# Performance work log

Hardware: AMD Instinct MI355X
Metric: run time of the kernel (lower is better)

## Reference

```python
import jax, jax.numpy as jnp
import numpy as np
import math


def setup_inputs() -> dict:
    key = jax.random.key(0)
    B, H, CL, QL = 16, 128, 2048, 256
    k0, k1, k2 = jax.random.split(key, 3)
    context = jax.random.normal(k0, (B, H, CL), dtype=jnp.float32)
    question = jax.random.normal(k1, (B, H, QL), dtype=jnp.float32)
    c_mask = jnp.ones((B, CL), dtype=jnp.int32)
    q_mask = jnp.ones((B, QL), dtype=jnp.int32)
    lim = math.sqrt(1.0 / H)
    w = jax.random.uniform(k2, (3 * H,), minval=-lim, maxval=lim, dtype=jnp.float32)
    return {"context": context, "question": question, "c_mask": c_mask, "q_mask": q_mask, "w": w}


def reference(context, question, c_mask, q_mask, w):
    # context: (B, H, c_len), question: (B, H, q_len), w: (3H,)
    H = context.shape[1]
    ctx = jnp.transpose(context, (0, 2, 1))   # (B, c_len, H)
    qry = jnp.transpose(question, (0, 2, 1))  # (B, q_len, H)
    wq, wc, wcq = w[:H], w[H:2 * H], w[2 * H:]
    # Trilinear similarity computed directly (no (B,c,q,3H) materialization):
    # s[b,i,j] = wq.q_j + wc.c_i + wcq.(c_i*q_j); torch layout after transpose is (B, c_len, q_len)
    s = (ctx @ wc)[:, :, None] + (qry @ wq)[:, None, :] + jnp.einsum('bch,bqh->bcq', ctx * wcq, qry)
    NEG = jnp.float32(-1e30)
    s1 = jax.nn.softmax(jnp.where(q_mask[:, None, :] > 0, s, NEG), axis=2)  # softmax over q
    s2 = jax.nn.softmax(jnp.where(c_mask[:, :, None] > 0, s, NEG), axis=1)  # softmax over c
    a = jnp.einsum('bcq,bqh->bch', s1, qry)          # context-to-query attention
    l = jnp.einsum('bcq,bkq->bck', s1, s2)           # s1 @ s2^T, (B, c_len, c_len)
    b = jnp.einsum('bck,bkh->bch', l, ctx)           # query-to-context attention
    out = jnp.concatenate([ctx, a, ctx * a, ctx * b], axis=2)  # (B, c_len, 4H)
    # drop_prob=0 -> dropout is identity
    return jnp.transpose(out, (0, 2, 1))  # (B, 4H, c_len)
```

## Files before the change

### kernel.cpp

```cpp
#include <hip/hip_runtime.h>

typedef short bf16x8 __attribute__((ext_vector_type(8)));
typedef float f32x16 __attribute__((ext_vector_type(16)));
typedef float f32x4  __attribute__((ext_vector_type(4)));

constexpr int B  = 16;
constexpr int H  = 128;
constexpr int CL = 2048;
constexpr int QL = 256;
constexpr int SPLITK5 = 8;
constexpr int K5SEG = CL / SPLITK5;
constexpr float SHIFT = 8.0f;

__device__ __forceinline__ unsigned short f2bf(float x) {
  unsigned u = __float_as_uint(x);
  u += 0x7fffu + ((u >> 16) & 1u);
  return (unsigned short)(u >> 16);
}
__device__ __forceinline__ float bf2f(unsigned short u) {
  return __uint_as_float((unsigned)u << 16);
}

template<int L, bool SCALE, bool WOUT, bool CM>
__device__ __forceinline__ void ktrans_body(
    const float* __restrict__ src, const float* __restrict__ wbias,
    const float* __restrict__ wscale, const int* __restrict__ cmask,
    unsigned short* __restrict__ dlin, unsigned short* __restrict__ dT,
    unsigned short* __restrict__ dm,
    float* __restrict__ pbias, float* __restrict__ outg0,
    int bxl, int h1, int b, int tid,
    unsigned short (*T)[72], float (*P)[64]) {
  const int c0 = bxl * 64;
  const int hh = tid >> 4;
  const int cc4 = (tid & 15) * 4;
  int4 cm4;
  if (CM) cm4 = *(const int4*)&cmask[b * L + c0 + cc4];
  float4 part = make_float4(0.f, 0.f, 0.f, 0.f);
  #pragma unroll
  for (int it = 0; it < 4; ++it) {
    const int hrow = it * 16 + hh;
    const int h = h1 * 64 + hrow;
    float4 v = *(const float4*)&src[((size_t)b * H + h) * L + c0 + cc4];
    const float wb = wbias[h];
    part.x = fmaf(v.x, wb, part.x); part.y = fmaf(v.y, wb, part.y);
    part.z = fmaf(v.z, wb, part.z); part.w = fmaf(v.w, wb, part.w);
    if (WOUT) {
      f32x4 t;
      t[0] = v.x; t[1] = v.y; t[2] = v.z; t[3] = v.w;
      __builtin_nontemporal_store(
          t, (f32x4*)&outg0[((size_t)b * 4 * H + h) * (size_t)CL + c0 + cc4]);
    }
    ushort4 o;
    o.x = f2bf(v.x); o.y = f2bf(v.y); o.z = f2bf(v.z); o.w = f2bf(v.w);
    *(ushort4*)&dlin[((size_t)b * H + h) * L + c0 + cc4] = o;
    if (CM) {
      ushort4 om;
      om.x = cm4.x > 0 ? o.x : (unsigned short)0;
      om.y = cm4.y > 0 ? o.y : (unsigned short)0;
      om.z = cm4.z > 0 ? o.z : (unsigned short)0;
      om.w = cm4.w > 0 ? o.w : (unsigned short)0;
      *(ushort4*)&dm[((size_t)b * H + h) * L + c0 + cc4] = om;
    }
    ushort4 ot;
    if (SCALE) {
      const float ws = wscale[h];
      ot.x = f2bf(v.x * ws); ot.y = f2bf(v.y * ws);
      ot.z = f2bf(v.z * ws); ot.w = f2bf(v.w * ws);
    } else {
      ot = o;
    }
    *(ushort4*)&T[hrow][cc4] = ot;
  }
  *(float4*)&P[hh][cc4] = part;
  __syncthreads();
  if (tid < 64) {
    float sum = 0.f;
    #pragma unroll
    for (int i = 0; i < 16; ++i) sum += P[i][tid];
    pbias[(size_t)h1 * B * L + (size_t)b * L + c0 + tid] = sum;
  }
  #pragma unroll
  for (int it = 0; it < 4; ++it) {
    int lin = it * 256 + tid;
    int c = lin >> 4, hc = (lin & 15) * 4;
    ushort4 o;
    o.x = T[hc + 0][c]; o.y = T[hc + 1][c];
    o.z = T[hc + 2][c]; o.w = T[hc + 3][c];
    *(ushort4*)&dT[((size_t)b * L + c0 + c) * H + h1 * 64 + hc] = o;
  }
}

__global__ __launch_bounds__(256) void ktrans_all(
    const float* __restrict__ ctx, const float* __restrict__ qry,
    const float* __restrict__ w, const int* __restrict__ cmask,
    unsigned short* __restrict__ ctx_bf, unsigned short* __restrict__ ctxwT,
    unsigned short* __restrict__ ctxm,
    unsigned short* __restrict__ qry_bf, unsigned short* __restrict__ qryT,
    float* __restrict__ pct, float* __restrict__ pqt,
    float* __restrict__ out) {
  __shared__ unsigned short T[64][72];
  __shared__ float P[16][64];
  const int h1 = blockIdx.y, b = blockIdx.z, tid = threadIdx.x;
  const int bx = blockIdx.x;
  if (bx < CL / 64) {
    ktrans_body<CL, true, true, true>(ctx, w + H, w + 2 * H, cmask,
                                      ctx_bf, ctxwT, ctxm, pct, out,
                                      bx, h1, b, tid, T, P);
  } else {
    ktrans_body<QL, false, false, false>(qry, w, w, nullptr,
                                         qry_bf, qryT, nullptr, pqt, nullptr,
                                         bx - CL / 64, h1, b, tid, T, P);
  }
}

__global__ __launch_bounds__(512) void k2_score3(
    const unsigned short* __restrict__ ctxwT, const unsigned short* __restrict__ qryT,
    const float* __restrict__ pct, const float* __restrict__ pqt,
    const int* __restrict__ cmask, const int* __restrict__ qmask,
    unsigned short* __restrict__ eu,
    float* __restrict__ rsum_g, float* __restrict__ Lpart) {
  __shared__ unsigned short t2[256 * 40];
  __shared__ float stats[32][8];
  __shared__ float cmf[32];
  const int wg = blockIdx.x;
  const int b = wg & (B - 1);
  const int cblk = wg >> 4;
  const int c0 = cblk * 32;
  const int tid = threadIdx.x;
  const int w = tid >> 6;
  const int l = tid & 63;
  const int lr = l & 31, hi = l >> 5;
  const int q0 = w * 32;
  const int c = c0 + lr;

  if (tid < 32) cmf[tid] = cmask[b * CL + c0 + tid] > 0 ? 1.f : 0.f;

  const unsigned short* ap = qryT + ((size_t)b * QL + q0 + lr) * H + hi * 8;
  const unsigned short* bp = ctxwT + ((size_t)b * CL + c) * H + hi * 8;
  f32x16 acc = {};
  #pragma unroll
  for (int k = 0; k < H; k += 16) {
    bf16x8 af = *(const bf16x8*)(ap + k);
    bf16x8 bf_ = *(const bf16x8*)(bp + k);
    acc = __builtin_amdgcn_mfma_f32_32x32x16_bf16(af, bf_, acc, 0, 0, 0);
  }

  const float ct = pct[b * CL + c] + pct[B * CL + b * CL + c];

  float rs = 0.f;
  #pragma unroll
  for (int g = 0; g < 4; ++g) {
    const int qbase = q0 + 4 * hi + 8 * g;
    float4 qa = *(const float4*)&pqt[b * QL + qbase];
    float4 qb = *(const float4*)&pqt[B * QL + b * QL + qbase];
    int4 m4 = *(const int4*)&qmask[b * QL + qbase];
    float e0 = __expf(acc[4 * g + 0] + ct + qa.x + qb.x - SHIFT);
    float e1 = __expf(acc[4 * g + 1] + ct + qa.y + qb.y - SHIFT);
    float e2 = __expf(acc[4 * g + 2] + ct + qa.z + qb.z - SHIFT);
    float e3 = __expf(acc[4 * g + 3] + ct + qa.w + qb.w - SHIFT);
    rs += (m4.x > 0 ? e0 : 0.f) + (m4.y > 0 ? e1 : 0.f) +
          (m4.z > 0 ? e2 : 0.f) + (m4.w > 0 ? e3 : 0.f);
    t2[(qbase + 0) * 40 + lr] = f2bf(e0);
    t2[(qbase + 1) * 40 + lr] = f2bf(e1);
    t2[(qbase + 2) * 40 + lr] = f2bf(e2);
    t2[(qbase + 3) * 40 + lr] = f2bf(e3);
  }
  rs += __shfl_xor(rs, 32);
  if (hi == 0) stats[lr][w] = rs;
  __syncthreads();

  if (tid < 32) {
    float s = 0.f;
    #pragma unroll
    for (int ww = 0; ww < 8; ++ww) s += stats[tid][ww];
    rsum_g[b * CL + c0 + tid] = s;
  }
  {
    const int q = tid >> 1, co = (tid & 1) * 16;
    bf16x8 v0 = *(const bf16x8*)&t2[q * 40 + co];
    bf16x8 v1 = *(const bf16x8*)&t2[q * 40 + co + 8];
    float cs = 0.f;
    #pragma unroll
    for (int i2 = 0; i2 < 8; ++i2) {
      cs += bf2f((unsigned short)v0[i2]) * cmf[co + i2];
      cs += bf2f((unsigned short)v1[i2]) * cmf[co + 8 + i2];
    }
    cs += __shfl_xor(cs, 1);
    unsigned short* op = eu + ((size_t)b * QL + q) * CL + c0 + co;
    *(bf16x8*)op = v0;
    *(bf16x8*)(op + 8) = v1;
    if ((tid & 1) == 0) Lpart[((size_t)b * 64 + cblk) * QL + q] = cs;
  }
}

__global__ __launch_bounds__(256, 4) void k5_tpart(
    const unsigned short* __restrict__ eu,
    const unsigned short* __restrict__ ctxm,
    unsigned short* __restrict__ tpart) {
  const int wg = blockIdx.x;
  const int b = wg & (B - 1);
  const int seg = (wg >> 4) & (SPLITK5 - 1);
  const int q0 = (wg >> 7) * 32;
  const int w = threadIdx.x >> 6, l = threadIdx.x & 63;
  const int h0 = w * 32;
  const int lr = l & 31, lg = l >> 5;
  const unsigned short* ap = eu + ((size_t)b * QL + q0 + lr) * CL + seg * K5SEG + lg * 8;
  const unsigned short* bp = ctxm + ((size_t)b * H + h0 + lr) * CL + seg * K5SEG + lg * 8;
  f32x16 acc = {};
  #pragma unroll
  for (int k = 0; k < K5SEG; k += 16) {
    bf16x8 af = *(const bf16x8*)(ap + k);
    bf16x8 bfr = *(const bf16x8*)(bp + k);
    acc = __builtin_amdgcn_mfma_f32_32x32x16_bf16(af, bfr, acc, 0, 0, 0);
  }
  unsigned short* tp = tpart + (size_t)(seg * B + b) * QL * H;
  #pragma unroll
  for (int r = 0; r < 16; ++r) {
    int qrow = (r & 3) + 8 * (r >> 2) + 4 * lg;
    tp[(size_t)(q0 + qrow) * H + h0 + lr] = f2bf(acc[r]);
  }
}

__global__ __launch_bounds__(256) void k5b_treduce(
    const unsigned short* __restrict__ tpart, const float* __restrict__ Lpart,
    unsigned short* __restrict__ tTbf) {
  __shared__ unsigned short lds[32 * 66];
  __shared__ float csum[4][64];
  __shared__ float cinv_s[64];
  const int q0 = blockIdx.x * 64, h0 = blockIdx.y * 32, b = blockIdx.z;
  const int tid = threadIdx.x;
  {
    const int qq = tid & 63, part = tid >> 6;
    float Ls = 0.f;
    #pragma unroll
    for (int k = 0; k < 16; ++k)
      Ls += Lpart[((size_t)b * 64 + part * 16 + k) * QL + q0 + qq];
    csum[part][qq] = Ls;
  }
  __syncthreads();
  if (tid < 64)
    cinv_s[tid] = 1.0f / (csum[0][tid] + csum[1][tid] + csum[2][tid] + csum[3][tid]);
  __syncthreads();
  for (int lin = tid; lin < 64 * 32; lin += 256) {
    int q = lin >> 5, h = lin & 31;
    float v = 0.f;
    #pragma unroll
    for (int sgt = 0; sgt < SPLITK5; ++sgt)
      v += bf2f(tpart[((size_t)(sgt * B + b) * QL + q0 + q) * H + h0 + h]);
    lds[h * 66 + q] = f2bf(v * cinv_s[q]);
  }
  __syncthreads();
  for (int lin = tid; lin < 32 * 64; lin += 256) {
    int h = lin >> 6, q = lin & 63;
    tTbf[((size_t)b * H + h0 + h) * QL + q0 + q] = lds[h * 66 + q];
  }
}

__device__ __forceinline__ int qswz(int q, int c) {
  return q ^ (((c >> 3) & 7) << 3);
}

__global__ __launch_bounds__(512) void kb_out(
    const unsigned short* __restrict__ eu,
    const unsigned short* __restrict__ qrybf, const unsigned short* __restrict__ tTbf,
    const unsigned short* __restrict__ ctxbf, const float* __restrict__ rsum_g,
    const int* __restrict__ qmask, float* __restrict__ out) {
  __shared__ unsigned short Ps[64 * 264];
  const int wg = blockIdx.x;
  const int b = wg & (B - 1);
  const int c0 = (wg >> 4) * 64;
  const int tid = threadIdx.x;
  const int w = tid >> 6, l = tid & 63;
  const int lr = l & 31, hi = l >> 5;
  const int h0 = (w & 3) * 32;
  const int ch = (w >> 2) * 32;
  const int c = c0 + ch + lr;

  #pragma unroll
  for (int p = 0; p < 4; ++p) {
    const int lin = p * 512 + tid;
    const int q = lin >> 3, co8 = (lin & 7) * 8;
    bf16x8 v = *(const bf16x8*)&eu[((size_t)b * QL + q) * CL + c0 + co8];
    const bool qm = qmask[b * QL + q] > 0;
    #pragma unroll
    for (int i = 0; i < 8; ++i) {
      const int cc = co8 + i;
      Ps[cc * 264 + qswz(q, cc)] = qm ? (unsigned short)v[i] : (unsigned short)0;
    }
  }

  const float rinv = 1.0f / rsum_g[b * CL + c];

  unsigned short cvu[16];
  {
    const unsigned short* cvp = ctxbf + (size_t)b * H * CL + c;
    #pragma unroll
    for (int r = 0; r < 16; ++r) {
      const int h = h0 + (r & 3) + 8 * (r >> 2) + 4 * hi;
      cvu[r] = cvp[(size_t)h * CL];
    }
  }
  __syncthreads();

  const unsigned short* a1p = qrybf + ((size_t)b * H + h0 + lr) * QL + hi * 8;
  const unsigned short* a2p = tTbf + ((size_t)b * H + h0 + lr) * QL + hi * 8;
  const int crow = ch + lr;
  f32x16 accA = {}, accB = {};
  #pragma unroll
  for (int kc = 0; kc < 16; ++kc) {
    bf16x8 pb = *(const bf16x8*)&Ps[crow * 264 + qswz(kc * 16 + hi * 8, crow)];
    bf16x8 a1 = *(const bf16x8*)(a1p + kc * 16);
    bf16x8 a2 = *(const bf16x8*)(a2p + kc * 16);
    accA = __builtin_amdgcn_mfma_f32_32x32x16_bf16(a1, pb, accA, 0, 0, 0);
    accB = __builtin_amdgcn_mfma_f32_32x32x16_bf16(a2, pb, accB, 0, 0, 0);
  }
  float* ob = out + (size_t)b * 4 * H * CL;
  #pragma unroll
  for (int r = 0; r < 16; ++r) {
    const int h = h0 + (r & 3) + 8 * (r >> 2) + 4 * hi;
    const float cv = bf2f(cvu[r]);
    const float av = accA[r] * rinv;
    const float bv = accB[r] * rinv;
    __builtin_nontemporal_store(av, &ob[(size_t)(H + h) * CL + c]);
    __builtin_nontemporal_store(cv * av, &ob[(size_t)(2 * H + h) * CL + c]);
    __builtin_nontemporal_store(cv * bv, &ob[(size_t)(3 * H + h) * CL + c]);
  }
}

extern "C" void kernel_launch(void* const* d_in, const int* in_sizes, int n_in,
                              void* d_out, int out_size, void* d_ws, size_t ws_size,
                              hipStream_t stream) {
  const float* context  = (const float*)d_in[0];
  const float* question = (const float*)d_in[1];
  const int*   c_mask   = (const int*)d_in[2];
  const int*   q_mask   = (const int*)d_in[3];
  const float* w        = (const float*)d_in[4];
  float* out = (float*)d_out;

  char* ws = (char*)d_ws;
  size_t off = 0;
  auto alloc = [&](size_t bytes) -> void* {
    void* p = ws + off;
    off += (bytes + 255) & ~(size_t)255;
    return p;
  };
  unsigned short* ctx_bf = (unsigned short*)alloc((size_t)B * H * CL * 2);
  unsigned short* ctxwT  = (unsigned short*)alloc((size_t)B * CL * H * 2);
  unsigned short* ctxm   = (unsigned short*)alloc((size_t)B * H * CL * 2);
  unsigned short* qry_bf = (unsigned short*)alloc((size_t)B * H * QL * 2);
  unsigned short* qryT   = (unsigned short*)alloc((size_t)B * QL * H * 2);
  unsigned short* eu     = (unsigned short*)alloc((size_t)B * QL * CL * 2);
  unsigned short* tpart  = (unsigned short*)alloc((size_t)SPLITK5 * B * QL * H * 2);
  unsigned short* tT_bf  = (unsigned short*)alloc((size_t)B * H * QL * 2);
  float* pct   = (float*)alloc((size_t)2 * B * CL * sizeof(float));
  float* pqt   = (float*)alloc((size_t)2 * B * QL * sizeof(float));
  float* rsum_ = (float*)alloc((size_t)B * CL * sizeof(float));
  float* Lpart = (float*)alloc((size_t)B * 64 * QL * sizeof(float));

  ktrans_all<<<dim3(CL / 64 + QL / 64, H / 64, B), dim3(256), 0, stream>>>(
      context, question, w, c_mask, ctx_bf, ctxwT, ctxm, qry_bf, qryT,
      pct, pqt, out);

  k2_score3<<<dim3((CL / 32) * B), dim3(512), 0, stream>>>(
      ctxwT, qryT, pct, pqt, c_mask, q_mask, eu, rsum_, Lpart);

  k5_tpart<<<dim3((QL / 32) * SPLITK5 * B), dim3(256), 0, stream>>>(
      eu, ctxm, tpart);

  k5b_treduce<<<dim3(QL / 64, H / 32, B), dim3(256), 0, stream>>>(
      tpart, Lpart, tT_bf);

  kb_out<<<dim3((CL / 64) * B), dim3(512), 0, stream>>>(
      eu, qry_bf, tT_bf, ctx_bf, rsum_, q_mask, out);
}
```

Measured before the change: 86.96 us.

## Drop masked context copy; apply masks in-register and bake q-mask into scores

Removes the separate c-mask-applied bf16 copy of the context (4 MB write plus 4 MB read). The c-mask is instead applied in k5 as a bitmask AND on the eu operand, built in LDS per segment. The q-mask is folded into the exponentials stored in eu, so kb_out no longer reloads or applies q_mask. The treduce grid is also halved per block (16 h rows instead of 32) to raise parallelism. This adds a little per-iteration LDS and ALU work in the k5 inner loop.

```diff
diff --git a/kernel.cpp b/kernel.cpp
--- a/kernel.cpp
+++ b/kernel.cpp
@@ -3,6 +3,7 @@
 typedef short bf16x8 __attribute__((ext_vector_type(8)));
 typedef float f32x16 __attribute__((ext_vector_type(16)));
 typedef float f32x4  __attribute__((ext_vector_type(4)));
+typedef unsigned int u32x4 __attribute__((ext_vector_type(4)));
 
 constexpr int B  = 16;
 constexpr int H  = 128;
@@ -21,20 +22,17 @@
   return __uint_as_float((unsigned)u << 16);
 }
 
-template<int L, bool SCALE, bool WOUT, bool CM>
+template<int L, bool SCALE, bool WOUT>
 __device__ __forceinline__ void ktrans_body(
     const float* __restrict__ src, const float* __restrict__ wbias,
-    const float* __restrict__ wscale, const int* __restrict__ cmask,
+    const float* __restrict__ wscale,
     unsigned short* __restrict__ dlin, unsigned short* __restrict__ dT,
-    unsigned short* __restrict__ dm,
     float* __restrict__ pbias, float* __restrict__ outg0,
     int bxl, int h1, int b, int tid,
     unsigned short (*T)[72], float (*P)[64]) {
   const int c0 = bxl * 64;
   const int hh = tid >> 4;
   const int cc4 = (tid & 15) * 4;
-  int4 cm4;
-  if (CM) cm4 = *(const int4*)&cmask[b * L + c0 + cc4];
   float4 part = make_float4(0.f, 0.f, 0.f, 0.f);
   #pragma unroll
   for (int it = 0; it < 4; ++it) {
@@ -53,14 +51,6 @@
     ushort4 o;
     o.x = f2bf(v.x); o.y = f2bf(v.y); o.z = f2bf(v.z); o.w = f2bf(v.w);
     *(ushort4*)&dlin[((size_t)b * H + h) * L + c0 + cc4] = o;
-    if (CM) {
-      ushort4 om;
-      om.x = cm4.x > 0 ? o.x : (unsigned short)0;
-      om.y = cm4.y > 0 ? o.y : (unsigned short)0;
-      om.z = cm4.z > 0 ? o.z : (unsigned short)0;
-      om.w = cm4.w > 0 ? o.w : (unsigned short)0;
-      *(ushort4*)&dm[((size_t)b * H + h) * L + c0 + cc4] = om;
-    }
     ushort4 ot;
     if (SCALE) {
       const float ws = wscale[h];
@@ -92,9 +82,8 @@
 
 __global__ __launch_bounds__(256) void ktrans_all(
     const float* __restrict__ ctx, const float* __restrict__ qry,
-    const float* __restrict__ w, const int* __restrict__ cmask,
+    const float* __restrict__ w,
     unsigned short* __restrict__ ctx_bf, unsigned short* __restrict__ ctxwT,
-    unsigned short* __restrict__ ctxm,
     unsigned short* __restrict__ qry_bf, unsigned short* __restrict__ qryT,
     float* __restrict__ pct, float* __restrict__ pqt,
     float* __restrict__ out) {
@@ -103,17 +92,15 @@
   const int h1 = blockIdx.y, b = blockIdx.z, tid = threadIdx.x;
   const int bx = blockIdx.x;
   if (bx < CL / 64) {
-    ktrans_body<CL, true, true, true>(ctx, w + H, w + 2 * H, cmask,
-                                      ctx_bf, ctxwT, ctxm, pct, out,
-                                      bx, h1, b, tid, T, P);
+    ktrans_body<CL, true, true>(ctx, w + H, w + 2 * H, ctx_bf, ctxwT, pct, out,
+                                bx, h1, b, tid, T, P);
   } else {
-    ktrans_body<QL, false, false, false>(qry, w, w, nullptr,
-                                         qry_bf, qryT, nullptr, pqt, nullptr,
-                                         bx - CL / 64, h1, b, tid, T, P);
-  }
-}
-
-__global__ __launch_bounds__(512) void k2_score3(
+    ktrans_body<QL, false, false>(qry, w, w, qry_bf, qryT, pqt, nullptr,
+                                  bx - CL / 64, h1, b, tid, T, P);
+  }
+}
+
+__global__ __launch_bounds__(512) void k2_score4(
     const unsigned short* __restrict__ ctxwT, const unsigned short* __restrict__ qryT,
     const float* __restrict__ pct, const float* __restrict__ pqt,
     const int* __restrict__ cmask, const int* __restrict__ qmask,
@@ -154,12 +141,11 @@
     float4 qa = *(const float4*)&pqt[b * QL + qbase];
     float4 qb = *(const float4*)&pqt[B * QL + b * QL + qbase];
     int4 m4 = *(const int4*)&qmask[b * QL + qbase];
-    float e0 = __expf(acc[4 * g + 0] + ct + qa.x + qb.x - SHIFT);
-    float e1 = __expf(acc[4 * g + 1] + ct + qa.y + qb.y - SHIFT);
-    float e2 = __expf(acc[4 * g + 2] + ct + qa.z + qb.z - SHIFT);
-    float e3 = __expf(acc[4 * g + 3] + ct + qa.w + qb.w - SHIFT);
-    rs += (m4.x > 0 ? e0 : 0.f) + (m4.y > 0 ? e1 : 0.f) +
-          (m4.z > 0 ? e2 : 0.f) + (m4.w > 0 ? e3 : 0.f);
+    float e0 = m4.x > 0 ? __expf(acc[4 * g + 0] + ct + qa.x + qb.x - SHIFT) : 0.f;
+    float e1 = m4.y > 0 ? __expf(acc[4 * g + 1] + ct + qa.y + qb.y - SHIFT) : 0.f;
+    float e2 = m4.z > 0 ? __expf(acc[4 * g + 2] + ct + qa.z + qb.z - SHIFT) : 0.f;
+    float e3 = m4.w > 0 ? __expf(acc[4 * g + 3] + ct + qa.w + qb.w - SHIFT) : 0.f;
+    rs += e0 + e1 + e2 + e3;
     t2[(qbase + 0) * 40 + lr] = f2bf(e0);
     t2[(qbase + 1) * 40 + lr] = f2bf(e1);
     t2[(qbase + 2) * 40 + lr] = f2bf(e2);
@@ -195,22 +181,35 @@
 
 __global__ __launch_bounds__(256, 4) void k5_tpart(
     const unsigned short* __restrict__ eu,
-    const unsigned short* __restrict__ ctxm,
+    const unsigned short* __restrict__ ctxbf,
+    const int* __restrict__ cmask,
     unsigned short* __restrict__ tpart) {
+  __shared__ unsigned int cmm[K5SEG / 2];
   const int wg = blockIdx.x;
   const int b = wg & (B - 1);
   const int seg = (wg >> 4) & (SPLITK5 - 1);
   const int q0 = (wg >> 7) * 32;
-  const int w = threadIdx.x >> 6, l = threadIdx.x & 63;
+  const int tid = threadIdx.x;
+  if (tid < K5SEG / 2) {
+    const int cbase = b * CL + seg * K5SEG + tid * 2;
+    cmm[tid] = (cmask[cbase] > 0 ? 0xFFFFu : 0u) |
+               (cmask[cbase + 1] > 0 ? 0xFFFF0000u : 0u);
+  }
+  __syncthreads();
+  const int w = tid >> 6, l = tid & 63;
   const int h0 = w * 32;
   const int lr = l & 31, lg = l >> 5;
   const unsigned short* ap = eu + ((size_t)b * QL + q0 + lr) * CL + seg * K5SEG + lg * 8;
-  const unsigned short* bp = ctxm + ((size_t)b * H + h0 + lr) * CL + seg * K5SEG + lg * 8;
+  const unsigned short* bp = ctxbf + ((size_t)b * H + h0 + lr) * CL + seg * K5SEG + lg * 8;
   f32x16 acc = {};
   #pragma unroll
   for (int k = 0; k < K5SEG; k += 16) {
     bf16x8 af = *(const bf16x8*)(ap + k);
     bf16x8 bfr = *(const bf16x8*)(bp + k);
+    u32x4 mm = *(const u32x4*)&cmm[(k >> 1) + lg * 4];
+    u32x4 ai = __builtin_bit_cast(u32x4, af);
+    ai &= mm;
+    af = __builtin_bit_cast(bf16x8, ai);
     acc = __builtin_amdgcn_mfma_f32_32x32x16_bf16(af, bfr, acc, 0, 0, 0);
   }
   unsigned short* tp = tpart + (size_t)(seg * B + b) * QL * H;
@@ -224,10 +223,10 @@
 __global__ __launch_bounds__(256) void k5b_treduce(
     const unsigned short* __restrict__ tpart, const float* __restrict__ Lpart,
     unsigned short* __restrict__ tTbf) {
-  __shared__ unsigned short lds[32 * 66];
+  __shared__ unsigned short lds[16 * 66];
   __shared__ float csum[4][64];
   __shared__ float cinv_s[64];
-  const int q0 = blockIdx.x * 64, h0 = blockIdx.y * 32, b = blockIdx.z;
+  const int q0 = blockIdx.x * 64, h0 = blockIdx.y * 16, b = blockIdx.z;
   const int tid = threadIdx.x;
   {
     const int qq = tid & 63, part = tid >> 6;
@@ -241,8 +240,8 @@
   if (tid < 64)
     cinv_s[tid] = 1.0f / (csum[0][tid] + csum[1][tid] + csum[2][tid] + csum[3][tid]);
   __syncthreads();
-  for (int lin = tid; lin < 64 * 32; lin += 256) {
-    int q = lin >> 5, h = lin & 31;
+  for (int lin = tid; lin < 64 * 16; lin += 256) {
+    int q = lin >> 4, h = lin & 15;
     float v = 0.f;
     #pragma unroll
     for (int sgt = 0; sgt < SPLITK5; ++sgt)
@@ -250,7 +249,7 @@
     lds[h * 66 + q] = f2bf(v * cinv_s[q]);
   }
   __syncthreads();
-  for (int lin = tid; lin < 32 * 64; lin += 256) {
+  for (int lin = tid; lin < 16 * 64; lin += 256) {
     int h = lin >> 6, q = lin & 63;
     tTbf[((size_t)b * H + h0 + h) * QL + q0 + q] = lds[h * 66 + q];
   }
@@ -264,7 +263,7 @@
     const unsigned short* __restrict__ eu,
     const unsigned short* __restrict__ qrybf, const unsigned short* __restrict__ tTbf,
     const unsigned short* __restrict__ ctxbf, const float* __restrict__ rsum_g,
-    const int* __restrict__ qmask, float* __restrict__ out) {
+    float* __restrict__ out) {
   __shared__ unsigned short Ps[64 * 264];
   const int wg = blockIdx.x;
   const int b = wg & (B - 1);
@@ -281,11 +280,10 @@
     const int lin = p * 512 + tid;
     const int q = lin >> 3, co8 = (lin & 7) * 8;
     bf16x8 v = *(const bf16x8*)&eu[((size_t)b * QL + q) * CL + c0 + co8];
-    const bool qm = qmask[b * QL + q] > 0;
     #pragma unroll
     for (int i = 0; i < 8; ++i) {
       const int cc = co8 + i;
-      Ps[cc * 264 + qswz(q, cc)] = qm ? (unsigned short)v[i] : (unsigned short)0;
+      Ps[cc * 264 + qswz(q, cc)] = (unsigned short)v[i];
     }
   }
 
@@ -346,7 +344,6 @@
   };
   unsigned short* ctx_bf = (unsigned short*)alloc((size_t)B * H * CL * 2);
   unsigned short* ctxwT  = (unsigned short*)alloc((size_t)B * CL * H * 2);
-  unsigned short* ctxm   = (unsigned short*)alloc((size_t)B * H * CL * 2);
   unsigned short* qry_bf = (unsigned short*)alloc((size_t)B * H * QL * 2);
   unsigned short* qryT   = (unsigned short*)alloc((size_t)B * QL * H * 2);
   unsigned short* eu     = (unsigned short*)alloc((size_t)B * QL * CL * 2);
@@ -358,18 +355,17 @@
   float* Lpart = (float*)alloc((size_t)B * 64 * QL * sizeof(float));
 
   ktrans_all<<<dim3(CL / 64 + QL / 64, H / 64, B), dim3(256), 0, stream>>>(
-      context, question, w, c_mask, ctx_bf, ctxwT, ctxm, qry_bf, qryT,
-      pct, pqt, out);
-
-  k2_score3<<<dim3((CL / 32) * B), dim3(512), 0, stream>>>(
+      context, question, w, ctx_bf, ctxwT, qry_bf, qryT, pct, pqt, out);
+
+  k2_score4<<<dim3((CL / 32) * B), dim3(512), 0, stream>>>(
       ctxwT, qryT, pct, pqt, c_mask, q_mask, eu, rsum_, Lpart);
 
   k5_tpart<<<dim3((QL / 32) * SPLITK5 * B), dim3(256), 0, stream>>>(
-      eu, ctxm, tpart);
-
-  k5b_treduce<<<dim3(QL / 64, H / 32, B), dim3(256), 0, stream>>>(
+      eu, ctx_bf, c_mask, tpart);
+
+  k5b_treduce<<<dim3(QL / 64, H / 16, B), dim3(256), 0, stream>>>(
       tpart, Lpart, tT_bf);
 
   kb_out<<<dim3((CL / 64) * B), dim3(512), 0, stream>>>(
-      eu, qry_bf, tT_bf, ctx_bf, rsum_, q_mask, out);
-}
+      eu, qry_bf, tT_bf, ctx_bf, rsum_, out);
+}
```

Result: faster. 85.25 us (-2.0%).
